# Kernel tuning notes

Hardware: AMD Instinct MI355X
Metric: run time of the kernel (lower is better)

## Reference

```python
import jax, jax.numpy as jnp
import numpy as np
from jax import lax

T, B, D, H, L = 256, 64, 512, 1024, 2


def _lstm_params(key):
    k = 1.0 / np.sqrt(H)
    params = {}
    in_dims = [D] + [H] * (L - 1)
    for l in range(L):
        key, k1, k2, k3, k4 = jax.random.split(key, 5)
        params[f"W_ih{l}"] = jax.random.uniform(k1, (4 * H, in_dims[l]), jnp.float32, -k, k)
        params[f"W_hh{l}"] = jax.random.uniform(k2, (4 * H, H), jnp.float32, -k, k)
        params[f"b_ih{l}"] = jax.random.uniform(k3, (4 * H,), jnp.float32, -k, k)
        params[f"b_hh{l}"] = jax.random.uniform(k4, (4 * H,), jnp.float32, -k, k)
    return params


def setup_inputs() -> dict:
    key = jax.random.key(0)
    k_in, k_rst, k_p = jax.random.split(key, 3)
    inp = {
        "input": jax.random.normal(k_in, (T, B, D), jnp.float32),
        "reset": jax.random.randint(k_rst, (T, B), 0, 2, jnp.int32),
        "h0": jnp.zeros((B, L, H), jnp.float32),
        "c0": jnp.zeros((B, L, H), jnp.float32),
    }
    inp.update(_lstm_params(k_p))
    return inp


def _run(input, reset_f, h0, c0, Wi, Wh, bi, bh):
    # state: [L, B, H]
    h = jnp.transpose(h0, (1, 0, 2))
    c = jnp.transpose(c0, (1, 0, 2))

    def step(carry, xt):
        h, c = carry
        x_t, r_t = xt  # x_t: [B, D], r_t: [B]
        keep = (1.0 - r_t)[None, :, None]  # reset gate zeroes state where reset==1
        h = h * keep
        c = c * keep
        x = x_t
        hs, cs = [], []
        for l in range(L):
            # gate order in torch nn.LSTM: i, f, g, o
            gates = x @ Wi[l].T + bi[l] + h[l] @ Wh[l].T + bh[l]
            i_g, f_g, g_g, o_g = jnp.split(gates, 4, axis=-1)
            c_new = jax.nn.sigmoid(f_g) * c[l] + jax.nn.sigmoid(i_g) * jnp.tanh(g_g)
            h_new = jax.nn.sigmoid(o_g) * jnp.tanh(c_new)
            hs.append(h_new)
            cs.append(c_new)
            x = h_new
        return (jnp.stack(hs), jnp.stack(cs)), x

    (h, c), outputs = lax.scan(step, (h, c), (input, reset_f))
    # back to [B, L, H] as in the torch module's returned state
    return outputs, jnp.transpose(h, (1, 0, 2)), jnp.transpose(c, (1, 0, 2))


def reference(input, reset, h0, c0, W_ih0, W_hh0, b_ih0, b_hh0, W_ih1, W_hh1, b_ih1, b_hh1):
    reset_f = reset.astype(jnp.float32)
    Wi = [W_ih0, W_ih1]
    Wh = [W_hh0, W_hh1]
    bi = [b_ih0, b_ih1]
    bh = [b_hh0, b_hh1]
    outputs, hN, cN = _run(input, reset_f, h0, c0, Wi, Wh, bi, bh)
    return outputs, (hN, cN)
```

## Files before the change

### kernel.cpp

```cpp
#include <hip/hip_runtime.h>

typedef __bf16 bf16x8 __attribute__((ext_vector_type(8)));
typedef float f32x4 __attribute__((ext_vector_type(4)));
typedef unsigned u32x4 __attribute__((ext_vector_type(4)));
typedef unsigned short u16;

constexpr int T = 256, B = 64, D = 512, H = 1024;
constexpr int G4 = 4 * H;
constexpr int NBLK = 256;
constexpr int NTHR = 256;
constexpr int BS = 32;
constexpr int MT = 2;

__device__ __forceinline__ u16 f2bf(float f) {
  unsigned u = __builtin_bit_cast(unsigned, f);
  u += 0x7fffu + ((u >> 16) & 1u);
  return (u16)(u >> 16);
}

__device__ __forceinline__ f32x4 mfma16(bf16x8 a, bf16x8 b, f32x4 c) {
  return __builtin_amdgcn_mfma_f32_16x16x32_bf16(a, b, c, 0, 0, 0);
}

__device__ __forceinline__ float sigm(float x) { return 1.f / (1.f + expf(-x)); }

__device__ __forceinline__ int ldflag(const int* f, int i) {
  return __hip_atomic_load(&f[i], __ATOMIC_RELAXED, __HIP_MEMORY_SCOPE_AGENT);
}

__global__ void cvt_bf16(const float* __restrict__ src, u16* __restrict__ dst, int n4) {
  int i = blockIdx.x * blockDim.x + threadIdx.x;
  int st = gridDim.x * blockDim.x;
  for (; i < n4; i += st) {
    float4 v = reinterpret_cast<const float4*>(src)[i];
    ushort4 o;
    o.x = f2bf(v.x); o.y = f2bf(v.y); o.z = f2bf(v.z); o.w = f2bf(v.w);
    reinterpret_cast<ushort4*>(dst)[i] = o;
  }
}

__global__ void init_state(const float* __restrict__ h0,
                           u16* __restrict__ xs1, u16* __restrict__ h1buf,
                           const float* __restrict__ bih0, const float* __restrict__ bhh0,
                           const float* __restrict__ bih1, const float* __restrict__ bhh1,
                           float* __restrict__ bias0, float* __restrict__ bias1,
                           int* __restrict__ flags) {
  int i = blockIdx.x * blockDim.x + threadIdx.x;
  if (i < NBLK) flags[i] = 0;
  if (i < 2 * B * H) {
    int l = i / (B * H), rem = i % (B * H);
    int b = rem / H, k = rem % H;
    u16 v = f2bf(h0[(size_t)b * 2 * H + (size_t)l * H + k]);
    if (l == 0) xs1[(size_t)b * H + k] = v;
    else        h1buf[(size_t)b * H + k] = v;
  }
  if (i < G4) {
    bias0[i] = bih0[i] + bhh0[i];
    bias1[i] = bih1[i] + bhh1[i];
  }
}

template <int L>
__device__ __forceinline__ void run_layer(
    const u16* __restrict__ xin, const u16* __restrict__ wx, const u16* __restrict__ wh,
    const float* __restrict__ bias, u16* __restrict__ xs1, u16* __restrict__ h1b,
    const float* __restrict__ c0, const int* __restrict__ reset,
    float* __restrict__ out, int* __restrict__ flags, int half, int col0,
    f32x4* __restrict__ red, unsigned* __restrict__ rbits, float* __restrict__ lbias,
    const int s1mask, const int h1mask, const int full) {
  constexpr int KX   = L ? H : D;
  constexpr int NCX  = KX / 32;
  constexpr int NCXW = NCX / 4;
  constexpr int NHW  = (H / 32) / 4;
  constexpr int NCW  = NCXW + NHW;
  const size_t BH = (size_t)B * H;
  const size_t OUT_HN = (size_t)T * BH;
  const size_t OUT_CN = OUT_HN + 2 * BH;

  const int tid  = threadIdx.x;
  const int ks   = tid >> 6;
  const int lane = tid & 63;
  const int q    = lane >> 4;
  const int ln   = lane & 15;

  for (int t = tid; t < T; t += NTHR) {
    unsigned v = 0;
#pragma unroll 8
    for (int i = 0; i < 32; ++i)
      v |= (unsigned)(reset[t * B + half * BS + i] & 1) << i;
    rbits[t] = v;
  }
  if (tid < 64) lbias[tid] = bias[(tid >> 4) * H + col0 + (tid & 15)];

  u32x4 wreg[4][NCW];
#pragma unroll
  for (int g = 0; g < 4; ++g)
#pragma unroll
    for (int cc = 0; cc < NCW; ++cc) {
      const bool isx = cc < NCXW;
      const int c = isx ? ks * NCXW + cc : ks * NHW + (cc - NCXW);
      const u16* W = isx ? wx : wh;
      const int stride = isx ? KX : H;
      const int kk = c * 32 + q * 8;
      wreg[g][cc] = *reinterpret_cast<const u32x4*>(
          W + (size_t)(g * H + col0 + ln) * stride + kk);
    }
#pragma unroll
  for (int g = 0; g < 4; ++g)
#pragma unroll
    for (int cc = 0; cc < NCW; ++cc)
      asm volatile("" : "+a"(wreg[g][cc]));

  const int b0l = (tid >> 4) * 4;
  const int cl  = col0 + (tid & 15);
  float creg[4] = {0.f, 0.f, 0.f, 0.f};
  if (tid < 128)
#pragma unroll
    for (int r = 0; r < 4; ++r)
      creg[r] = c0[(size_t)(half * BS + b0l + r) * 2 * H + (size_t)L * H + cl];

  __syncthreads();
  float bval[4];
#pragma unroll
  for (int g = 0; g < 4; ++g) bval[g] = lbias[g * 16 + (tid & 15)];

  float hv[4] = {0.f, 0.f, 0.f, 0.f};

  uint4 xf[NCXW][MT];
  auto load_xfrags = [&](const u16* xsrc) {
#pragma unroll
    for (int cc = 0; cc < NCXW; ++cc) {
      const int kk = (ks * NCXW + cc) * 32 + q * 8;
#pragma unroll
      for (int m = 0; m < MT; ++m)
        xf[cc][m] = *reinterpret_cast<const uint4*>(
            xsrc + (size_t)(half * BS + 16 * m + ln) * KX + kk);
    }
  };
  if (full && L == 0) load_xfrags(xin);

  for (int s = 0; s <= T; ++s) {
    const bool active = (L == 0) ? (s < T) : (s >= 1);
    const int t = (L == 0) ? s : s - 1;
    if (active) {
      if (full) {
        const int gbase = L * 128 + half * 64;
        while (ldflag(flags, gbase + lane) < s) __builtin_amdgcn_s_sleep(1);
        asm volatile("" ::: "memory");
      } else {
        for (;;) {
          int a = ldflag(flags, lane),       b = ldflag(flags, 64 + lane);
          int c = ldflag(flags, 128 + lane), d = ldflag(flags, 192 + lane);
          int m1 = a < b ? a : b, m2 = c < d ? c : d;
          if ((m1 < m2 ? m1 : m2) >= s) break;
          __builtin_amdgcn_s_sleep(1);
        }
        __builtin_amdgcn_fence(__ATOMIC_ACQUIRE, "agent");
        asm volatile("" ::: "memory");
        const u16* xsrc = (L == 0) ? xin + (size_t)t * B * D
                                   : xs1 + (size_t)(s & s1mask) * BH;
        load_xfrags(xsrc);
      }

      const u16* hsrc = (L == 0) ? xs1 + (size_t)(s & s1mask) * BH
                                 : h1b + (size_t)(t & h1mask) * BH;
      uint4 hf[NHW][MT];
#pragma unroll
      for (int cc = 0; cc < NHW; ++cc) {
        const int kk = (ks * NHW + cc) * 32 + q * 8;
#pragma unroll
        for (int m = 0; m < MT; ++m)
          hf[cc][m] = *reinterpret_cast<const uint4*>(
              hsrc + (size_t)(half * BS + 16 * m + ln) * H + kk);
      }

      f32x4 acc[4][MT];
#pragma unroll
      for (int g = 0; g < 4; ++g)
#pragma unroll
        for (int m = 0; m < MT; ++m) acc[g][m] = (f32x4){0.f, 0.f, 0.f, 0.f};

#pragma unroll
      for (int cc = 0; cc < NCXW; ++cc)
#pragma unroll
        for (int g = 0; g < 4; ++g)
#pragma unroll
          for (int m = 0; m < MT; ++m)
            acc[g][m] = mfma16(__builtin_bit_cast(bf16x8, xf[cc][m]),
                               __builtin_bit_cast(bf16x8, wreg[g][cc]), acc[g][m]);

      const unsigned rw = rbits[t];
      const int rz0 = (int)((rw >> ln) & 1u);
      const int rz1 = (int)((rw >> (16 + ln)) & 1u);
      const uint4 zz = make_uint4(0u, 0u, 0u, 0u);
#pragma unroll
      for (int cc = 0; cc < NHW; ++cc) {
        const uint4 v0 = rz0 ? zz : hf[cc][0];
        const uint4 v1 = rz1 ? zz : hf[cc][1];
#pragma unroll
        for (int g = 0; g < 4; ++g) {
          acc[g][0] = mfma16(__builtin_bit_cast(bf16x8, v0),
                             __builtin_bit_cast(bf16x8, wreg[g][NCXW + cc]), acc[g][0]);
          acc[g][1] = mfma16(__builtin_bit_cast(bf16x8, v1),
                             __builtin_bit_cast(bf16x8, wreg[g][NCXW + cc]), acc[g][1]);
        }
      }

#pragma unroll
      for (int g = 0; g < 4; ++g)
#pragma unroll
        for (int m = 0; m < MT; ++m)
          red[(g * 4 + ks) * (MT * 64) + m * 64 + lane] = acc[g][m];
      __syncthreads();

      if (tid < 128) {
        f32x4 gate[4];
#pragma unroll
        for (int g = 0; g < 4; ++g) {
          f32x4 sum = red[(g * 4 + 0) * (MT * 64) + tid];
#pragma unroll
          for (int w = 1; w < 4; ++w) sum += red[(g * 4 + w) * (MT * 64) + tid];
          gate[g] = sum + (f32x4){bval[g], bval[g], bval[g], bval[g]};
        }
        const unsigned rstw = rbits[t] >> b0l;
        u16 hb[4];
#pragma unroll
        for (int r = 0; r < 4; ++r) {
          float cp = ((rstw >> r) & 1u) ? 0.f : creg[r];
          float i_ = sigm(gate[0][r]);
          float f_ = sigm(gate[1][r]);
          float g_ = tanhf(gate[2][r]);
          float o_ = sigm(gate[3][r]);
          float cn = fmaf(f_, cp, i_ * g_);
          float hn = o_ * tanhf(cn);
          creg[r] = cn;
          hv[r] = hn;
          hb[r] = f2bf(hn);
        }
        u16* hdst = (L == 0)
            ? xs1 + (size_t)((s + 1) & s1mask) * BH
            : h1b + (size_t)((t + 1) & h1mask) * BH;
#pragma unroll
        for (int r = 0; r < 4; ++r) {
          unsigned own = hb[r];
          unsigned oth = (unsigned)__shfl_xor((int)own, 1);
          unsigned pk = (tid & 1) ? ((oth & 0xffffu) | (own << 16))
                                  : (own | (oth << 16));
          if ((r >> 1) == (tid & 1))
            __hip_atomic_store(
                reinterpret_cast<unsigned*>(
                    hdst + (size_t)(half * BS + b0l + r) * H + (cl & ~1)),
                pk, __ATOMIC_RELAXED, __HIP_MEMORY_SCOPE_AGENT);
        }
        if (t == T - 1) {
#pragma unroll
          for (int r = 0; r < 4; ++r) {
            const size_t brow = (size_t)(half * BS + b0l + r);
            __builtin_nontemporal_store(
                hv[r], &out[OUT_HN + brow * 2 * H + (size_t)L * H + cl]);
            __builtin_nontemporal_store(
                creg[r], &out[OUT_CN + brow * 2 * H + (size_t)L * H + cl]);
            if (L == 1)
              __builtin_nontemporal_store(
                  hv[r], &out[(size_t)t * BH + brow * H + cl]);
          }
        }
      }
    }

    if (s < T) {
      __syncthreads();
      if (tid == 0)
        __hip_atomic_store(&flags[blockIdx.x], s + 1,
                           __ATOMIC_RELAXED, __HIP_MEMORY_SCOPE_AGENT);
      if (L == 1 && active && t < T - 1 && tid < 128) {
#pragma unroll
        for (int r = 0; r < 4; ++r)
          __builtin_nontemporal_store(
              hv[r], &out[(size_t)t * BH + (size_t)(half * BS + b0l + r) * H + cl]);
      }
      if (full) {
        if (L == 0) {
          if (s + 1 < T) load_xfrags(xin + (size_t)(s + 1) * B * D);
        } else {
          while (ldflag(flags, half * 64 + lane) < s + 1) __builtin_amdgcn_s_sleep(1);
          asm volatile("" ::: "memory");
          load_xfrags(xs1 + (size_t)((s + 1) & s1mask) * BH);
        }
      }
    }
  }
}

__global__ void __launch_bounds__(NTHR, 1) lstm_seq(
    const u16* __restrict__ xin,
    const u16* __restrict__ wx0, const u16* __restrict__ wh0,
    const u16* __restrict__ wx1, const u16* __restrict__ wh1,
    const float* __restrict__ bias0, const float* __restrict__ bias1,
    u16* __restrict__ xs1, u16* __restrict__ h1b,
    const float* __restrict__ c0, const int* __restrict__ reset,
    float* __restrict__ out, int* __restrict__ flags,
    int s1mask, int h1mask, int full) {
  __shared__ f32x4 red[4 * 4 * MT * 64];
  __shared__ unsigned rbits[T];
  __shared__ float lbias[64];
  const int group = blockIdx.x >> 7;
  const int half  = (blockIdx.x >> 6) & 1;
  const int col0  = (blockIdx.x & 63) << 4;
  if (group == 0)
    run_layer<0>(xin, wx0, wh0, bias0, xs1, h1b, c0, reset, out, flags, half, col0,
                 red, rbits, lbias, s1mask, h1mask, full);
  else
    run_layer<1>(nullptr, wx1, wh1, bias1, xs1, h1b, c0, reset, out, flags, half, col0,
                 red, rbits, lbias, s1mask, h1mask, full);
}

extern "C" void kernel_launch(void* const* d_in, const int* in_sizes, int n_in,
                              void* d_out, int out_size, void* d_ws, size_t ws_size,
                              hipStream_t stream) {
  (void)in_sizes; (void)n_in; (void)out_size;
  const float* input = (const float*)d_in[0];
  const int*   reset = (const int*)d_in[1];
  const float* h0    = (const float*)d_in[2];
  const float* c0    = (const float*)d_in[3];
  const float* Wih0  = (const float*)d_in[4];
  const float* Whh0  = (const float*)d_in[5];
  const float* bih0  = (const float*)d_in[6];
  const float* bhh0  = (const float*)d_in[7];
  const float* Wih1  = (const float*)d_in[8];
  const float* Whh1  = (const float*)d_in[9];
  const float* bih1  = (const float*)d_in[10];
  const float* bhh1  = (const float*)d_in[11];
  float* out = (float*)d_out;
  char* ws = (char*)d_ws;

  const size_t SLOT = (size_t)B * H * 2;
  const size_t FIXED = (size_t)G4 * D * 2 + 3 * (size_t)G4 * H * 2
                     + (size_t)T * B * D * 2
                     + 2 * (size_t)G4 * 4 + 4096;
  const bool full = ws_size >= FIXED + 2 * (size_t)(T + 1) * SLOT + 65536;
  const int d0 = full ? (T + 1) : 4;
  const int d1 = full ? (T + 1) : 2;
  const int s1mask = full ? 511 : 3;
  const int h1mask = full ? 511 : 1;

  size_t off = 0;
  auto alloc = [&](size_t bytes) { size_t o = off; off += (bytes + 255) & ~(size_t)255; return o; };
  u16* wx0 = (u16*)(ws + alloc((size_t)G4 * D * 2));
  u16* wh0 = (u16*)(ws + alloc((size_t)G4 * H * 2));
  u16* wx1 = (u16*)(ws + alloc((size_t)G4 * H * 2));
  u16* wh1 = (u16*)(ws + alloc((size_t)G4 * H * 2));
  u16* xin = (u16*)(ws + alloc((size_t)T * B * D * 2));
  u16* xs1 = (u16*)(ws + alloc((size_t)d0 * SLOT));
  u16* h1b = (u16*)(ws + alloc((size_t)d1 * SLOT));
  float* pb0 = (float*)(ws + alloc((size_t)G4 * 4));
  float* pb1 = (float*)(ws + alloc((size_t)G4 * 4));
  int* flg = (int*)(ws + alloc(1024));

  cvt_bf16<<<1024, 256, 0, stream>>>(Wih0, wx0, G4 * D / 4);
  cvt_bf16<<<1024, 256, 0, stream>>>(Whh0, wh0, G4 * H / 4);
  cvt_bf16<<<1024, 256, 0, stream>>>(Wih1, wx1, G4 * H / 4);
  cvt_bf16<<<1024, 256, 0, stream>>>(Whh1, wh1, G4 * H / 4);
  cvt_bf16<<<2048, 256, 0, stream>>>(input, xin, T * B * D / 4);
  init_state<<<512, 256, 0, stream>>>(h0, xs1, h1b, bih0, bhh0, bih1, bhh1, pb0, pb1, flg);
  lstm_seq<<<NBLK, NTHR, 0, stream>>>(xin, wx0, wh0, wx1, wh1, pb0, pb1,
                                      xs1, h1b, c0, reset, out, flg,
                                      s1mask, h1mask, full ? 1 : 0);
}
```

Measured before the change: 1.955 ms.

## Use per-wave flags with chunked dependency polling and fast activations in LSTM

Replaces the per-block step flags with per-wave flags, so each wave publishes its hidden-state slice right after writing it without a block-wide barrier. Consumers poll the flags of the producers of each K-chunk and issue those h loads as they become ready, overlapping the x-side MFMAs with waiting. It also double-buffers the reduction LDS buffer, remaps block indices for locality, and switches sigmoid/tanh to rcp/__expf approximations. The cost is more flag traffic and more complex polling, plus slightly lower activation precision.

Measured after the change: 2.344 ms. 19.9% more time.

```diff
diff --git a/kernel.cpp b/kernel.cpp
--- a/kernel.cpp
+++ b/kernel.cpp
@@ -22,7 +22,12 @@
   return __builtin_amdgcn_mfma_f32_16x16x32_bf16(a, b, c, 0, 0, 0);
 }
 
-__device__ __forceinline__ float sigm(float x) { return 1.f / (1.f + expf(-x)); }
+__device__ __forceinline__ float sigm(float x) {
+  return __builtin_amdgcn_rcpf(1.f + __expf(-x));
+}
+__device__ __forceinline__ float tanhfast(float x) {
+  return 1.f - 2.f * __builtin_amdgcn_rcpf(__expf(2.f * x) + 1.f);
+}
 
 __device__ __forceinline__ int ldflag(const int* f, int i) {
   return __hip_atomic_load(&f[i], __ATOMIC_RELAXED, __HIP_MEMORY_SCOPE_AGENT);
@@ -46,7 +51,7 @@
                            float* __restrict__ bias0, float* __restrict__ bias1,
                            int* __restrict__ flags) {
   int i = blockIdx.x * blockDim.x + threadIdx.x;
-  if (i < NBLK) flags[i] = 0;
+  if (i < 2 * NBLK) flags[i] = (i >= 2 * 128) ? 1 : 0;
   if (i < 2 * B * H) {
     int l = i / (B * H), rem = i % (B * H);
     int b = rem / H, k = rem % H;
@@ -65,7 +70,7 @@
     const u16* __restrict__ xin, const u16* __restrict__ wx, const u16* __restrict__ wh,
     const float* __restrict__ bias, u16* __restrict__ xs1, u16* __restrict__ h1b,
     const float* __restrict__ c0, const int* __restrict__ reset,
-    float* __restrict__ out, int* __restrict__ flags, int half, int col0,
+    float* __restrict__ out, int* __restrict__ flags, int half, int col0, int lb,
     f32x4* __restrict__ red, unsigned* __restrict__ rbits, float* __restrict__ lbias,
     const int s1mask, const int h1mask, const int full) {
   constexpr int KX   = L ? H : D;
@@ -124,8 +129,6 @@
 #pragma unroll
   for (int g = 0; g < 4; ++g) bval[g] = lbias[g * 16 + (tid & 15)];
 
-  float hv[4] = {0.f, 0.f, 0.f, 0.f};
-
   uint4 xf[NCXW][MT];
   auto load_xfrags = [&](const u16* xsrc) {
 #pragma unroll
@@ -139,39 +142,60 @@
   };
   if (full && L == 0) load_xfrags(xin);
 
+  const int fbaseH = 2 * ((L * 2 + half) * 64 + ks * 16);
+  const int fbaseX = 2 * (half * 64 + ks * 16);
+  int l0seen = 0;
+
   for (int s = 0; s <= T; ++s) {
     const bool active = (L == 0) ? (s < T) : (s >= 1);
     const int t = (L == 0) ? s : s - 1;
     if (active) {
-      if (full) {
-        const int gbase = L * 128 + half * 64;
-        while (ldflag(flags, gbase + lane) < s) __builtin_amdgcn_s_sleep(1);
-        asm volatile("" ::: "memory");
-      } else {
-        for (;;) {
-          int a = ldflag(flags, lane),       b = ldflag(flags, 64 + lane);
-          int c = ldflag(flags, 128 + lane), d = ldflag(flags, 192 + lane);
-          int m1 = a < b ? a : b, m2 = c < d ? c : d;
-          if ((m1 < m2 ? m1 : m2) >= s) break;
-          __builtin_amdgcn_s_sleep(1);
-        }
-        __builtin_amdgcn_fence(__ATOMIC_ACQUIRE, "agent");
-        asm volatile("" ::: "memory");
-        const u16* xsrc = (L == 0) ? xin + (size_t)t * B * D
-                                   : xs1 + (size_t)(s & s1mask) * BH;
-        load_xfrags(xsrc);
-      }
-
       const u16* hsrc = (L == 0) ? xs1 + (size_t)(s & s1mask) * BH
                                  : h1b + (size_t)(t & h1mask) * BH;
       uint4 hf[NHW][MT];
-#pragma unroll
-      for (int cc = 0; cc < NHW; ++cc) {
-        const int kk = (ks * NHW + cc) * 32 + q * 8;
-#pragma unroll
-        for (int m = 0; m < MT; ++m)
-          hf[cc][m] = *reinterpret_cast<const uint4*>(
-              hsrc + (size_t)(half * BS + 16 * m + ln) * H + kk);
+      unsigned issuedChunks = 0;
+
+      auto pollIssue = [&]() {
+        int fv = (lane < 32) ? ldflag(flags, fbaseH + lane) : 0x7fffffff;
+        unsigned rdy = (unsigned)__ballot(fv >= s);
+        asm volatile("" ::: "memory");
+        unsigned newly = 0;
+#pragma unroll
+        for (int cc = 0; cc < NHW; ++cc)
+          if (((rdy >> (4 * cc)) & 0xFu) == 0xFu) newly |= 1u << cc;
+        newly &= ~issuedChunks;
+#pragma unroll
+        for (int cc = 0; cc < NHW; ++cc)
+          if ((newly >> cc) & 1u) {
+            const int kk = (ks * NHW + cc) * 32 + q * 8;
+            hf[cc][0] = *reinterpret_cast<const uint4*>(
+                hsrc + (size_t)(half * BS + ln) * H + kk);
+            hf[cc][1] = *reinterpret_cast<const uint4*>(
+                hsrc + (size_t)(half * BS + 16 + ln) * H + kk);
+          }
+        issuedChunks |= newly;
+      };
+
+      if (full) {
+        pollIssue();
+      } else {
+        while (ldflag(flags, tid) < s || ldflag(flags, 256 + tid) < s)
+          __builtin_amdgcn_s_sleep(1);
+        __syncthreads();
+        if (tid == 0) __builtin_amdgcn_fence(__ATOMIC_ACQUIRE, "agent");
+        __syncthreads();
+        asm volatile("" ::: "memory");
+        load_xfrags((L == 0) ? xin + (size_t)t * B * D
+                             : xs1 + (size_t)(s & s1mask) * BH);
+#pragma unroll
+        for (int cc = 0; cc < NHW; ++cc) {
+          const int kk = (ks * NHW + cc) * 32 + q * 8;
+          hf[cc][0] = *reinterpret_cast<const uint4*>(
+              hsrc + (size_t)(half * BS + ln) * H + kk);
+          hf[cc][1] = *reinterpret_cast<const uint4*>(
+              hsrc + (size_t)(half * BS + 16 + ln) * H + kk);
+        }
+        issuedChunks = (1u << NHW) - 1u;
       }
 
       f32x4 acc[4][MT];
@@ -188,6 +212,12 @@
           for (int m = 0; m < MT; ++m)
             acc[g][m] = mfma16(__builtin_bit_cast(bf16x8, xf[cc][m]),
                                __builtin_bit_cast(bf16x8, wreg[g][cc]), acc[g][m]);
+
+      if (full)
+        while (issuedChunks != (1u << NHW) - 1u) {
+          __builtin_amdgcn_s_sleep(1);
+          pollIssue();
+        }
 
       const unsigned rw = rbits[t];
       const int rz0 = (int)((rw >> ln) & 1u);
@@ -206,51 +236,55 @@
         }
       }
 
+      f32x4* rbuf = red + (size_t)(s & 1) * (16 * 128);
 #pragma unroll
       for (int g = 0; g < 4; ++g)
 #pragma unroll
         for (int m = 0; m < MT; ++m)
-          red[(g * 4 + ks) * (MT * 64) + m * 64 + lane] = acc[g][m];
+          rbuf[(g * 4 + ks) * 128 + m * 64 + lane] = acc[g][m];
       __syncthreads();
 
       if (tid < 128) {
         f32x4 gate[4];
 #pragma unroll
         for (int g = 0; g < 4; ++g) {
-          f32x4 sum = red[(g * 4 + 0) * (MT * 64) + tid];
-#pragma unroll
-          for (int w = 1; w < 4; ++w) sum += red[(g * 4 + w) * (MT * 64) + tid];
+          f32x4 sum = rbuf[(g * 4 + 0) * 128 + tid];
+#pragma unroll
+          for (int w = 1; w < 4; ++w) sum += rbuf[(g * 4 + w) * 128 + tid];
           gate[g] = sum + (f32x4){bval[g], bval[g], bval[g], bval[g]};
         }
         const unsigned rstw = rbits[t] >> b0l;
+        float hv[4];
         u16 hb[4];
 #pragma unroll
         for (int r = 0; r < 4; ++r) {
           float cp = ((rstw >> r) & 1u) ? 0.f : creg[r];
           float i_ = sigm(gate[0][r]);
           float f_ = sigm(gate[1][r]);
-          float g_ = tanhf(gate[2][r]);
+          float g_ = tanhfast(gate[2][r]);
           float o_ = sigm(gate[3][r]);
           float cn = fmaf(f_, cp, i_ * g_);
-          float hn = o_ * tanhf(cn);
+          float hn = o_ * tanhfast(cn);
           creg[r] = cn;
           hv[r] = hn;
           hb[r] = f2bf(hn);
         }
-        u16* hdst = (L == 0)
-            ? xs1 + (size_t)((s + 1) & s1mask) * BH
-            : h1b + (size_t)((t + 1) & h1mask) * BH;
-#pragma unroll
-        for (int r = 0; r < 4; ++r) {
-          unsigned own = hb[r];
-          unsigned oth = (unsigned)__shfl_xor((int)own, 1);
-          unsigned pk = (tid & 1) ? ((oth & 0xffffu) | (own << 16))
-                                  : (own | (oth << 16));
-          if ((r >> 1) == (tid & 1))
-            __hip_atomic_store(
-                reinterpret_cast<unsigned*>(
-                    hdst + (size_t)(half * BS + b0l + r) * H + (cl & ~1)),
-                pk, __ATOMIC_RELAXED, __HIP_MEMORY_SCOPE_AGENT);
+        if (s < T) {
+          u16* hdst = (L == 0)
+              ? xs1 + (size_t)((s + 1) & s1mask) * BH
+              : h1b + (size_t)((t + 1) & h1mask) * BH;
+#pragma unroll
+          for (int r = 0; r < 4; ++r) {
+            unsigned own = hb[r];
+            unsigned oth = (unsigned)__shfl_xor((int)own, 1);
+            unsigned pk = (tid & 1) ? ((oth & 0xffffu) | (own << 16))
+                                    : (own | (oth << 16));
+            if ((r >> 1) == (tid & 1))
+              __hip_atomic_store(
+                  reinterpret_cast<unsigned*>(
+                      hdst + (size_t)(half * BS + b0l + r) * H + (cl & ~1)),
+                  pk, __ATOMIC_RELAXED, __HIP_MEMORY_SCOPE_AGENT);
+          }
         }
         if (t == T - 1) {
 #pragma unroll
@@ -265,27 +299,46 @@
                   hv[r], &out[(size_t)t * BH + brow * H + cl]);
           }
         }
+        if (full && s < T) {
+          asm volatile("s_waitcnt vmcnt(0)" ::: "memory");
+          if (lane == 0)
+            __hip_atomic_store(&flags[2 * lb + (tid >> 6)], s + 1,
+                               __ATOMIC_RELAXED, __HIP_MEMORY_SCOPE_AGENT);
+        }
+        if (L == 1 && t < T - 1) {
+#pragma unroll
+          for (int r = 0; r < 4; ++r)
+            out[(size_t)t * BH + (size_t)(half * BS + b0l + r) * H + cl] = hv[r];
+        }
       }
     }
 
     if (s < T) {
-      __syncthreads();
-      if (tid == 0)
-        __hip_atomic_store(&flags[blockIdx.x], s + 1,
-                           __ATOMIC_RELAXED, __HIP_MEMORY_SCOPE_AGENT);
-      if (L == 1 && active && t < T - 1 && tid < 128) {
-#pragma unroll
-        for (int r = 0; r < 4; ++r)
-          __builtin_nontemporal_store(
-              hv[r], &out[(size_t)t * BH + (size_t)(half * BS + b0l + r) * H + cl]);
-      }
       if (full) {
         if (L == 0) {
           if (s + 1 < T) load_xfrags(xin + (size_t)(s + 1) * B * D);
         } else {
-          while (ldflag(flags, half * 64 + lane) < s + 1) __builtin_amdgcn_s_sleep(1);
-          asm volatile("" ::: "memory");
+          if (l0seen <= s) {
+            for (;;) {
+              int fv = (lane < 32) ? ldflag(flags, fbaseX + lane) : 0x7fffffff;
+              int mn = fv;
+#pragma unroll
+              for (int o = 1; o < 64; o <<= 1) mn = min(mn, __shfl_xor(mn, o));
+              l0seen = mn;
+              if (l0seen >= s + 1) break;
+              __builtin_amdgcn_s_sleep(1);
+            }
+            asm volatile("" ::: "memory");
+          }
           load_xfrags(xs1 + (size_t)((s + 1) & s1mask) * BH);
+        }
+      } else {
+        __syncthreads();
+        if (tid == 0) {
+          __hip_atomic_store(&flags[2 * lb], s + 1,
+                             __ATOMIC_RELAXED, __HIP_MEMORY_SCOPE_AGENT);
+          __hip_atomic_store(&flags[2 * lb + 1], s + 1,
+                             __ATOMIC_RELAXED, __HIP_MEMORY_SCOPE_AGENT);
         }
       }
     }
@@ -301,17 +354,19 @@
     const float* __restrict__ c0, const int* __restrict__ reset,
     float* __restrict__ out, int* __restrict__ flags,
     int s1mask, int h1mask, int full) {
-  __shared__ f32x4 red[4 * 4 * MT * 64];
+  __shared__ f32x4 red[2 * 16 * 128];
   __shared__ unsigned rbits[T];
   __shared__ float lbias[64];
-  const int group = blockIdx.x >> 7;
-  const int half  = (blockIdx.x >> 6) & 1;
-  const int col0  = (blockIdx.x & 63) << 4;
-  if (group == 0)
-    run_layer<0>(xin, wx0, wh0, bias0, xs1, h1b, c0, reset, out, flags, half, col0,
+  const int g    = (blockIdx.x & 7) >> 1;
+  const int c    = ((blockIdx.x >> 3) << 1) | (blockIdx.x & 1);
+  const int half = g & 1;
+  const int col0 = c << 4;
+  const int lb   = g * 64 + c;
+  if ((g >> 1) == 0)
+    run_layer<0>(xin, wx0, wh0, bias0, xs1, h1b, c0, reset, out, flags, half, col0, lb,
                  red, rbits, lbias, s1mask, h1mask, full);
   else
-    run_layer<1>(nullptr, wx1, wh1, bias1, xs1, h1b, c0, reset, out, flags, half, col0,
+    run_layer<1>(nullptr, wx1, wh1, bias1, xs1, h1b, c0, reset, out, flags, half, col0, lb,
                  red, rbits, lbias, s1mask, h1mask, full);
 }
 
@@ -337,7 +392,7 @@
   const size_t SLOT = (size_t)B * H * 2;
   const size_t FIXED = (size_t)G4 * D * 2 + 3 * (size_t)G4 * H * 2
                      + (size_t)T * B * D * 2
-                     + 2 * (size_t)G4 * 4 + 4096;
+                     + 2 * (size_t)G4 * 4 + 8192;
   const bool full = ws_size >= FIXED + 2 * (size_t)(T + 1) * SLOT + 65536;
   const int d0 = full ? (T + 1) : 4;
   const int d1 = full ? (T + 1) : 2;
@@ -355,7 +410,7 @@
   u16* h1b = (u16*)(ws + alloc((size_t)d1 * SLOT));
   float* pb0 = (float*)(ws + alloc((size_t)G4 * 4));
   float* pb1 = (float*)(ws + alloc((size_t)G4 * 4));
-  int* flg = (int*)(ws + alloc(1024));
+  int* flg = (int*)(ws + alloc(2048));
 
   cvt_bf16<<<1024, 256, 0, stream>>>(Wih0, wx0, G4 * D / 4);
   cvt_bf16<<<1024, 256, 0, stream>>>(Whh0, wh0, G4 * H / 4);
```

## Narrow per-wave flag waits and remap blocks to interleave layers across XCDs

Applied to the files above, without the earlier changes.

Each wave now polls only the 16 producer flags for the K-slice it reads, instead of all 64 flags of a half. Layer 1 caches the minimum layer-0 progress it has already seen so it can skip repeated polling. Block-to-role mapping is permuted so the four groups (layer x half) interleave across block indices, likely spreading them over XCDs, and flags are indexed by logical block id. The last-step h store is skipped and the per-step output store becomes a normal store. This relies on the per-slice wait being enough for correctness, and on the remapping's effect on cache locality across XCDs.

After: 1.817 ms. -7.1%, faster.

```diff
diff --git a/kernel.cpp b/kernel.cpp
--- a/kernel.cpp
+++ b/kernel.cpp
@@ -65,7 +65,7 @@
     const u16* __restrict__ xin, const u16* __restrict__ wx, const u16* __restrict__ wh,
     const float* __restrict__ bias, u16* __restrict__ xs1, u16* __restrict__ h1b,
     const float* __restrict__ c0, const int* __restrict__ reset,
-    float* __restrict__ out, int* __restrict__ flags, int half, int col0,
+    float* __restrict__ out, int* __restrict__ flags, int half, int col0, int lb,
     f32x4* __restrict__ red, unsigned* __restrict__ rbits, float* __restrict__ lbias,
     const int s1mask, const int h1mask, const int full) {
   constexpr int KX   = L ? H : D;
@@ -139,13 +139,18 @@
   };
   if (full && L == 0) load_xfrags(xin);
 
+  const int gbase = (L * 2 + half) * 64 + ks * 16;
+  const int xbase = half * 64 + ks * 16;
+  int l0seen = 0;
+
   for (int s = 0; s <= T; ++s) {
     const bool active = (L == 0) ? (s < T) : (s >= 1);
     const int t = (L == 0) ? s : s - 1;
     if (active) {
+      const u16* hsrc = (L == 0) ? xs1 + (size_t)(s & s1mask) * BH
+                                 : h1b + (size_t)(t & h1mask) * BH;
       if (full) {
-        const int gbase = L * 128 + half * 64;
-        while (ldflag(flags, gbase + lane) < s) __builtin_amdgcn_s_sleep(1);
+        while (ldflag(flags, gbase + (lane & 15)) < s) __builtin_amdgcn_s_sleep(1);
         asm volatile("" ::: "memory");
       } else {
         for (;;) {
@@ -157,13 +162,10 @@
         }
         __builtin_amdgcn_fence(__ATOMIC_ACQUIRE, "agent");
         asm volatile("" ::: "memory");
-        const u16* xsrc = (L == 0) ? xin + (size_t)t * B * D
-                                   : xs1 + (size_t)(s & s1mask) * BH;
-        load_xfrags(xsrc);
-      }
-
-      const u16* hsrc = (L == 0) ? xs1 + (size_t)(s & s1mask) * BH
-                                 : h1b + (size_t)(t & h1mask) * BH;
+        load_xfrags((L == 0) ? xin + (size_t)t * B * D
+                             : xs1 + (size_t)(s & s1mask) * BH);
+      }
+
       uint4 hf[NHW][MT];
 #pragma unroll
       for (int cc = 0; cc < NHW; ++cc) {
@@ -237,20 +239,22 @@
           hv[r] = hn;
           hb[r] = f2bf(hn);
         }
-        u16* hdst = (L == 0)
-            ? xs1 + (size_t)((s + 1) & s1mask) * BH
-            : h1b + (size_t)((t + 1) & h1mask) * BH;
-#pragma unroll
-        for (int r = 0; r < 4; ++r) {
-          unsigned own = hb[r];
-          unsigned oth = (unsigned)__shfl_xor((int)own, 1);
-          unsigned pk = (tid & 1) ? ((oth & 0xffffu) | (own << 16))
-                                  : (own | (oth << 16));
-          if ((r >> 1) == (tid & 1))
-            __hip_atomic_store(
-                reinterpret_cast<unsigned*>(
-                    hdst + (size_t)(half * BS + b0l + r) * H + (cl & ~1)),
-                pk, __ATOMIC_RELAXED, __HIP_MEMORY_SCOPE_AGENT);
+        if (s < T) {
+          u16* hdst = (L == 0)
+              ? xs1 + (size_t)((s + 1) & s1mask) * BH
+              : h1b + (size_t)((t + 1) & h1mask) * BH;
+#pragma unroll
+          for (int r = 0; r < 4; ++r) {
+            unsigned own = hb[r];
+            unsigned oth = (unsigned)__shfl_xor((int)own, 1);
+            unsigned pk = (tid & 1) ? ((oth & 0xffffu) | (own << 16))
+                                    : (own | (oth << 16));
+            if ((r >> 1) == (tid & 1))
+              __hip_atomic_store(
+                  reinterpret_cast<unsigned*>(
+                      hdst + (size_t)(half * BS + b0l + r) * H + (cl & ~1)),
+                  pk, __ATOMIC_RELAXED, __HIP_MEMORY_SCOPE_AGENT);
+          }
         }
         if (t == T - 1) {
 #pragma unroll
@@ -271,20 +275,30 @@
     if (s < T) {
       __syncthreads();
       if (tid == 0)
-        __hip_atomic_store(&flags[blockIdx.x], s + 1,
+        __hip_atomic_store(&flags[lb], s + 1,
                            __ATOMIC_RELAXED, __HIP_MEMORY_SCOPE_AGENT);
       if (L == 1 && active && t < T - 1 && tid < 128) {
 #pragma unroll
         for (int r = 0; r < 4; ++r)
-          __builtin_nontemporal_store(
-              hv[r], &out[(size_t)t * BH + (size_t)(half * BS + b0l + r) * H + cl]);
+          out[(size_t)t * BH + (size_t)(half * BS + b0l + r) * H + cl] = hv[r];
       }
       if (full) {
         if (L == 0) {
           if (s + 1 < T) load_xfrags(xin + (size_t)(s + 1) * B * D);
         } else {
-          while (ldflag(flags, half * 64 + lane) < s + 1) __builtin_amdgcn_s_sleep(1);
-          asm volatile("" ::: "memory");
+          if (l0seen < s + 1) {
+            int fv;
+            for (;;) {
+              fv = ldflag(flags, xbase + (lane & 15));
+              if (__all(fv >= s + 1)) break;
+              __builtin_amdgcn_s_sleep(1);
+            }
+            int mn = fv;
+#pragma unroll
+            for (int o = 1; o < 64; o <<= 1) mn = min(mn, __shfl_xor(mn, o));
+            l0seen = mn;
+            asm volatile("" ::: "memory");
+          }
           load_xfrags(xs1 + (size_t)((s + 1) & s1mask) * BH);
         }
       }
@@ -304,14 +318,16 @@
   __shared__ f32x4 red[4 * 4 * MT * 64];
   __shared__ unsigned rbits[T];
   __shared__ float lbias[64];
-  const int group = blockIdx.x >> 7;
-  const int half  = (blockIdx.x >> 6) & 1;
-  const int col0  = (blockIdx.x & 63) << 4;
-  if (group == 0)
-    run_layer<0>(xin, wx0, wh0, bias0, xs1, h1b, c0, reset, out, flags, half, col0,
+  const int g    = (blockIdx.x & 7) >> 1;
+  const int c    = ((blockIdx.x >> 3) << 1) | (blockIdx.x & 1);
+  const int half = g & 1;
+  const int col0 = c << 4;
+  const int lb   = g * 64 + c;
+  if ((g >> 1) == 0)
+    run_layer<0>(xin, wx0, wh0, bias0, xs1, h1b, c0, reset, out, flags, half, col0, lb,
                  red, rbits, lbias, s1mask, h1mask, full);
   else
-    run_layer<1>(nullptr, wx1, wh1, bias1, xs1, h1b, c0, reset, out, flags, half, col0,
+    run_layer<1>(nullptr, wx1, wh1, bias1, xs1, h1b, c0, reset, out, flags, half, col0, lb,
                  red, rbits, lbias, s1mask, h1mask, full);
 }
 
@@ -337,7 +353,7 @@
   const size_t SLOT = (size_t)B * H * 2;
   const size_t FIXED = (size_t)G4 * D * 2 + 3 * (size_t)G4 * H * 2
                      + (size_t)T * B * D * 2
-                     + 2 * (size_t)G4 * 4 + 4096;
+                     + 2 * (size_t)G4 * 4 + 8192;
   const bool full = ws_size >= FIXED + 2 * (size_t)(T + 1) * SLOT + 65536;
   const int d0 = full ? (T + 1) : 4;
   const int d1 = full ? (T + 1) : 2;
```
